# Kernel tuning notes

Measured on AMD Instinct MI355X. Metric: run time of the kernel, lower is better.

The kernel has to match this reference:

```python
import jax, jax.numpy as jnp
from jax import lax
import numpy as np

EPS = 1e-12      # F.normalize eps
TOP_N = 250      # top negatives selected
SMOOTH = 1e-5    # soft dice smooth


def _dilate10(m):
    # == 10 iterations of 3x3x3 binary max-pool dilation. m: [B,D,H,W] float.
    for _ in range(10):
        m = lax.reduce_window(m, 0.0, lax.max, (1, 3, 3, 3), (1, 1, 1, 1), 'SAME')
    return m


def _self_loss(feature, lab):
    # feature: [B,C,D,H,W], lab: [B,D,H,W] int
    feat = jnp.moveaxis(feature, 1, -1)                       # [B,D,H,W,C]
    pos = (lab == 1)
    posf = pos.astype(feat.dtype)
    cnt = posf.sum()
    std = (feat * posf[..., None]).sum((0, 1, 2, 3)) / jnp.maximum(cnt, 1.0)
    std = jnp.where(cnt > 0, std, 0.0)                        # [C]
    std_n = std / jnp.maximum(jnp.linalg.norm(std), EPS)
    feat_n = feat / jnp.maximum(jnp.linalg.norm(feat, axis=-1, keepdims=True), EPS)
    # cosine similarity of per-voxel normalized features vs normalized mean positive
    sim = jnp.einsum('bdhwc,c->bdhw', feat_n, std_n)

    # positive term: mean over positives of (1 - sim)
    pos_loss = jnp.where(cnt > 0, ((1.0 - sim) * posf).sum() / jnp.maximum(cnt, 1.0), 0.0)

    # easily-misclassified ring: dilate(pos,10) & ~pos; mean relu(sim)
    mis = (_dilate10(posf) > 0) & (~pos)
    misf = mis.astype(sim.dtype)
    mcnt = misf.sum()
    mis_loss = jnp.where(mcnt > 0, (jax.nn.relu(sim) * misf).sum() / jnp.maximum(mcnt, 1.0), 0.0)

    # hard negatives: top-250 sims among label==0, scatter to mask, dilate, & ~pos
    neg = (lab == 0)
    neg_sims = jnp.where(neg, sim, -jnp.inf).reshape(-1)
    top_vals, top_idx = lax.top_k(neg_sims, TOP_N)
    hsm = jnp.zeros(neg_sims.shape[0], sim.dtype).at[top_idx].set(
        jnp.where(jnp.isfinite(top_vals), 1.0, 0.0)).reshape(sim.shape)
    fin = (_dilate10(hsm) > 0) & (~pos)
    finf = fin.astype(sim.dtype)
    fcnt = finf.sum()
    neg_loss = jnp.where(fcnt > 0, (jax.nn.relu(sim) * finf).sum() / jnp.maximum(fcnt, 1.0), 0.0)

    return pos_loss + mis_loss + neg_loss


def _ce_dice(net_output, target):
    lab = target[:, 0]                                        # [B,D,H,W]
    logp = jax.nn.log_softmax(net_output, axis=1)
    ce = -jnp.mean(jnp.take_along_axis(logp, target, axis=1))
    probs = jnp.exp(logp)                                     # softmax_helper_dim1
    nc = net_output.shape[1]
    onehot = jax.nn.one_hot(lab, nc, axis=1, dtype=probs.dtype)  # [B,nc,D,H,W]
    axes = (0, 2, 3, 4)                                       # batch_dice=True
    tp = (probs * onehot).sum(axes)
    fp = (probs * (1.0 - onehot)).sum(axes)
    fn = ((1.0 - probs) * onehot).sum(axes)
    dc = (2.0 * tp + SMOOTH) / (2.0 * tp + fp + fn + SMOOTH + 1e-8)
    dice = -jnp.mean(dc[1:])                                  # do_bg=False
    return ce, dice


def reference(feature, net_output, target):
    ce, dice = _ce_dice(net_output, target)
    sl = _self_loss(feature, target[:, 0])
    return 1.0 * ce + 1.0 * dice + 5.0 * sl


def setup_inputs():
    key = jax.random.key(0)
    k1, k2, k3 = jax.random.split(key, 3)
    B, C, D, H, W = 2, 32, 64, 128, 128
    NC = 2
    feature = jax.random.normal(k1, (B, C, D, H, W), jnp.float32)
    net_output = jax.random.normal(k2, (B, NC, D, H, W), jnp.float32)
    target = jax.random.randint(k3, (B, 1, D, H, W), 0, 2).astype(jnp.int32)
    return {'feature': feature, 'net_output': net_output, 'target': target}
```

## Files before the change

kernel.cpp:

```cpp
#include <hip/hip_runtime.h>
#include <stdint.h>

typedef unsigned int u32;
typedef unsigned long long u64;
typedef float f4v __attribute__((ext_vector_type(4)));
typedef int i4v __attribute__((ext_vector_type(4)));

#define BB 2
#define CC 32
#define DD 64
#define HH 128
#define WW 128
#define SS (DD*HH*WW)
#define NN (BB*SS)
#define NQ (NN/4)
#define NWORDS (NN/64)
#define EPSF 1e-12f
#define TOPN 250u

struct Ctrl {
  u32 done4, tie, pad0, pad1;
};

struct Acc {
  double ce, tp, fp, fn;
  double stdsum[CC];
  double pos_num, mis_num, fin_num;
  u64 cnt, mcnt, fcnt;
};

__device__ __forceinline__ float waveRedF(float v){
#pragma unroll
  for (int o = 32; o; o >>= 1) v += __shfl_xor(v, o);
  return v;
}
__device__ __forceinline__ u32 waveRedU(u32 v){
#pragma unroll
  for (int o = 32; o; o >>= 1) v += __shfl_xor(v, o);
  return v;
}
__device__ __forceinline__ void red_d(double* dst, float v, volatile float* sh){
  int lane = threadIdx.x & 63, wid = threadIdx.x >> 6;
  v = waveRedF(v);
  if (lane == 0) sh[wid] = v;
  __syncthreads();
  if (threadIdx.x == 0){
    float t = 0.f;
    for (int i = 0; i < (int)(blockDim.x >> 6); i++) t += sh[i];
    atomicAdd(dst, (double)t);
  }
  __syncthreads();
}
__device__ __forceinline__ void red_u(u64* dst, u32 v, volatile u32* sh){
  int lane = threadIdx.x & 63, wid = threadIdx.x >> 6;
  v = waveRedU(v);
  if (lane == 0) sh[wid] = v;
  __syncthreads();
  if (threadIdx.x == 0){
    u32 t = 0;
    for (int i = 0; i < (int)(blockDim.x >> 6); i++) t += sh[i];
    atomicAdd(dst, (u64)t);
  }
  __syncthreads();
}

__device__ __forceinline__ u32 sortkey(float f){
  u32 u = __float_as_uint(f);
  return (u & 0x80000000u) ? ~u : (u | 0x80000000u);
}

__device__ __forceinline__ void select_top(const u32* __restrict__ hist, u32 nbins,
                                           u32 k, u32* shres, u32* binOut, u32* kremOut){
  __syncthreads();
  if (threadIdx.x < 64){
    int lane = threadIdx.x;
    u32 running = 0; bool found = false;
    for (u32 chunk = 0; chunk * 64 < nbins && !found; chunk++){
      int bin = (int)nbins - 1 - (int)(chunk * 64 + (u32)lane);
      u32 val = (bin >= 0) ? hist[bin] : 0u;
      u32 p = val;
#pragma unroll
      for (int o = 1; o < 64; o <<= 1){ u32 t = __shfl_up(p, o); if (lane >= o) p += t; }
      u32 tot = __shfl(p, 63);
      u32 incl = running + p, excl = incl - val;
      bool hit = (excl < k) && (incl >= k);
      u64 mb = __ballot(hit);
      if (mb){
        int hl = __ffsll((unsigned long long)mb) - 1;
        if (lane == hl){ shres[0] = (u32)bin; shres[1] = k - excl; }
        found = true;
      } else running += tot;
    }
    if (!found && lane == 0){ shres[0] = 0; shres[1] = k; }
  }
  __syncthreads();
  *binOut = shres[0]; *kremOut = shres[1];
}

__global__ __launch_bounds__(256) void k_pre(const int* __restrict__ tgt,
                                             u64* __restrict__ pbits,
                                             u32* __restrict__ cntArr,
                                             u32* __restrict__ zptr, u32 zwords){
  __shared__ u32 nibsh[256];
  __shared__ u32 shu[4];
  if (blockIdx.x == 0){
    for (u32 i = threadIdx.x; i < zwords; i += 256u) zptr[i] = 0;
  }
  u32 cnt = 0;
#pragma unroll 1
  for (u32 it = 0; it < 4; it++){
    u32 q = blockIdx.x * 1024u + it * 256u + threadIdx.x;
    i4v l4 = __builtin_nontemporal_load((const i4v*)(tgt + q * 4u));
    u32 nib = (l4.x ? 1u : 0u) | (l4.y ? 2u : 0u) | (l4.z ? 4u : 0u) | (l4.w ? 8u : 0u);
    cnt += __popc(nib);
    __syncthreads();
    nibsh[threadIdx.x] = nib;
    __syncthreads();
    if (threadIdx.x < 16){
      u64 o = 0;
#pragma unroll
      for (int j = 0; j < 16; j++)
        o |= (u64)(nibsh[threadIdx.x * 16 + j] & 0xFu) << (4 * j);
      pbits[blockIdx.x * 64u + it * 16u + threadIdx.x] = o;
    }
  }
  int lane = threadIdx.x & 63, wid = threadIdx.x >> 6;
  cnt = waveRedU(cnt);
  if (lane == 0) shu[wid] = cnt;
  __syncthreads();
  if (threadIdx.x == 0) cntArr[blockIdx.x] = shu[0] + shu[1] + shu[2] + shu[3];
}

__global__ __launch_bounds__(256) void k_ce_std(const float* __restrict__ feat,
                                                const float* __restrict__ net,
                                                const u64* __restrict__ pbits, Acc* acc){
  __shared__ float sh[16];
  if (blockIdx.x < 64u){
    u32 bid = blockIdx.x;
    float ce = 0.f, tp = 0.f, fp = 0.f, fnn = 0.f;
#pragma unroll 1
    for (u32 it = 0; it < 32; it++){
      u32 q = bid * 8192u + it * 256u + threadIdx.x;
      u32 nib = (u32)(pbits[q >> 4] >> ((q & 15u) << 2)) & 0xFu;
      u32 v = q * 4u;
      u32 b = v >> 20, s = v & (SS - 1);
      const float* nb = net + (size_t)(b * 2) * SS + s;
      f4v x0 = __builtin_nontemporal_load((const f4v*)(nb));
      f4v x1 = __builtin_nontemporal_load((const f4v*)(nb + SS));
      float xs0[4] = {x0.x, x0.y, x0.z, x0.w};
      float xs1[4] = {x1.x, x1.y, x1.z, x1.w};
#pragma unroll
      for (int j = 0; j < 4; j++){
        int lab = (nib >> j) & 1;
        float m = fmaxf(xs0[j], xs1[j]);
        float lse = m + logf(expf(xs0[j] - m) + expf(xs1[j] - m));
        ce += lse - (lab ? xs1[j] : xs0[j]);
        float p1 = expf(xs1[j] - lse);
        if (lab){ tp += p1; fnn += 1.0f - p1; } else fp += p1;
      }
    }
    int lane = threadIdx.x & 63, wid = threadIdx.x >> 6;
    ce = waveRedF(ce); tp = waveRedF(tp); fp = waveRedF(fp); fnn = waveRedF(fnn);
    if (lane == 0){ sh[wid] = ce; sh[4 + wid] = tp; sh[8 + wid] = fp; sh[12 + wid] = fnn; }
    __syncthreads();
    if (threadIdx.x == 0){
      atomicAdd(&acc->ce, (double)(sh[0] + sh[1] + sh[2] + sh[3]));
      atomicAdd(&acc->tp, (double)(sh[4] + sh[5] + sh[6] + sh[7]));
      atomicAdd(&acc->fp, (double)(sh[8] + sh[9] + sh[10] + sh[11]));
      atomicAdd(&acc->fn, (double)(sh[12] + sh[13] + sh[14] + sh[15]));
    }
  } else {
    u32 bx = blockIdx.x - 64u;
    u32 c = bx & 31u;
    u32 chunk = bx >> 5;
    u32 vbase = chunk * 65536u;
    u32 b = vbase >> 20;
    u32 s0 = vbase & (SS - 1);
    const float* fp_ = feat + (size_t)b * CC * SS + (size_t)c * SS + s0;
    const u64* pb = pbits + (vbase >> 6);
    float a = 0.f;
#pragma unroll 8
    for (u32 i = 0; i < 64; i++){
      u32 off = i * 1024u + threadIdx.x * 4u;
      float4 f = *(const float4*)(fp_ + off);
      u32 bits = (u32)(pb[off >> 6] >> (off & 63u)) & 0xFu;
      if (bits & 1u) a += f.x;
      if (bits & 2u) a += f.y;
      if (bits & 4u) a += f.z;
      if (bits & 8u) a += f.w;
    }
    int lane = threadIdx.x & 63, wid = threadIdx.x >> 6;
    a = waveRedF(a);
    if (lane == 0) sh[wid] = a;
    __syncthreads();
    if (threadIdx.x == 0)
      atomicAdd(&acc->stdsum[c], (double)(sh[0] + sh[1] + sh[2] + sh[3]));
  }
}

__global__ __launch_bounds__(256) void k_sim(const float* __restrict__ feat,
                                             const u64* __restrict__ pbits,
                                             const u32* __restrict__ cntArr,
                                             Acc* acc, float* __restrict__ sim,
                                             u32* __restrict__ h1){
  __shared__ float st[CC];
  __shared__ u32 lh[2048];
  __shared__ float shf[4];
  __shared__ u32 scnt;
  if (threadIdx.x < 64){
    u32 sc = 0;
#pragma unroll
    for (int i = 0; i < 8; i++) sc += cntArr[threadIdx.x * 8 + i];
    sc = waveRedU(sc);
    if (threadIdx.x == 0) scnt = sc;
  }
  __syncthreads();
  u32 cnt = scnt;
  if (blockIdx.x == 0 && threadIdx.x == 0) acc->cnt = (u64)cnt;
  {
    float sv = 0.f;
    if (threadIdx.x < CC && cnt) sv = (float)(acc->stdsum[threadIdx.x] / (double)cnt);
    if (threadIdx.x < 64){
      float t = waveRedF(sv * sv);
      float d = fmaxf(sqrtf(t), EPSF);
      if (threadIdx.x < CC) st[threadIdx.x] = sv / d;
    }
  }
  for (u32 i = threadIdx.x; i < 2048u; i += 256u) lh[i] = 0;
  __syncthreads();
  u32 vbase = (511u - blockIdx.x) * 4096u;
  u32 b = vbase >> 20;
  u32 s0 = vbase & (SS - 1);
  const float* fp = feat + (size_t)b * CC * SS + s0;
  float4 dt[4], n2[4];
#pragma unroll
  for (int g = 0; g < 4; g++){
    dt[g].x = dt[g].y = dt[g].z = dt[g].w = 0.f;
    n2[g].x = n2[g].y = n2[g].z = n2[g].w = 0.f;
  }
#pragma unroll 2
  for (u32 c = 0; c < CC; c++){
    float w = st[c];
    const float* fc = fp + (size_t)c * SS;
    float4 f[4];
#pragma unroll
    for (int g = 0; g < 4; g++)
      f[g] = *(const float4*)(fc + (u32)g * 1024u + threadIdx.x * 4u);
#pragma unroll
    for (int g = 0; g < 4; g++){
      dt[g].x += f[g].x * w; dt[g].y += f[g].y * w;
      dt[g].z += f[g].z * w; dt[g].w += f[g].w * w;
      n2[g].x += f[g].x * f[g].x; n2[g].y += f[g].y * f[g].y;
      n2[g].z += f[g].z * f[g].z; n2[g].w += f[g].w * f[g].w;
    }
  }
  float pn = 0.f;
#pragma unroll
  for (int g = 0; g < 4; g++){
    u32 off = (u32)g * 1024u + threadIdx.x * 4u;
    u32 v = vbase + off;
    float4 sm;
    sm.x = dt[g].x / fmaxf(sqrtf(n2[g].x), EPSF);
    sm.y = dt[g].y / fmaxf(sqrtf(n2[g].y), EPSF);
    sm.z = dt[g].z / fmaxf(sqrtf(n2[g].z), EPSF);
    sm.w = dt[g].w / fmaxf(sqrtf(n2[g].w), EPSF);
    *(float4*)(sim + v) = sm;
    u32 bits = (u32)(pbits[v >> 6] >> (v & 63u)) & 0xFu;
    float ss[4] = {sm.x, sm.y, sm.z, sm.w};
#pragma unroll
    for (int j = 0; j < 4; j++){
      if ((bits >> j) & 1u) pn += 1.f - ss[j];
      else atomicAdd(&lh[sortkey(ss[j]) >> 21], 1u);
    }
  }
  __syncthreads();
  for (u32 i = threadIdx.x; i < 2048u; i += 256u)
    if (lh[i]) atomicAdd(&h1[i], lh[i]);
  red_d(&acc->pos_num, pn, shf);
}

__device__ __forceinline__ void dilwh_slab(const u64* __restrict__ in, u64* __restrict__ out,
                                           u32 slab, u64* arr){
  u32 base = slab * 256u;
  int t = threadIdx.x;
  if (t < 128){
    u64 lo = in[base + 2 * t], hi = in[base + 2 * t + 1];
    u64 al = lo, ah = hi;
#pragma unroll
    for (int i = 0; i < 10; i++){ u64 c = al >> 63; ah = ah | (ah << 1) | c; al = al | (al << 1); }
    u64 bl = lo, bh = hi;
#pragma unroll
    for (int i = 0; i < 10; i++){ u64 c = bh << 63; bl = bl | (bl >> 1) | c; bh = bh | (bh >> 1); }
    arr[2 * t] = al | bl;
    arr[2 * t + 1] = ah | bh;
  }
  __syncthreads();
  int h = t >> 1, wj = t & 1;
  int h0 = h - 10 > 0 ? h - 10 : 0;
  int h1 = h + 10 < 127 ? h + 10 : 127;
  u64 o = 0;
  for (int hh = h0; hh <= h1; hh++) o |= arr[2 * hh + wj];
  out[base + (u32)t] = o;
  __syncthreads();
}

__global__ __launch_bounds__(256) void k_dilwh(const u64* __restrict__ in, u64* __restrict__ out){
  __shared__ u64 arr[256];
  dilwh_slab(in, out, blockIdx.x, arr);
}

__global__ __launch_bounds__(256) void k_histL2(const float* __restrict__ sim,
                                                const u64* __restrict__ pbits,
                                                const u32* __restrict__ h1,
                                                u32* __restrict__ h2,
                                                const u64* __restrict__ P,
                                                u64* __restrict__ T1P){
  __shared__ u64 arr[256];
  __shared__ u32 lh[2048];
  __shared__ u32 shres[2];
  if (blockIdx.x < 128u) dilwh_slab(P, T1P, blockIdx.x, arr);
  u32 p1, k1;
  select_top(h1, 2048, TOPN, shres, &p1, &k1);
  for (u32 i = threadIdx.x; i < 2048u; i += 256u) lh[i] = 0;
  __syncthreads();
  const u32 stride = 512u * 256u;
#pragma unroll 1
  for (u32 it = 0; it < 4; it++){
    u32 q = blockIdx.x * 256u + threadIdx.x + it * stride;
    u32 nib = (u32)(pbits[q >> 4] >> ((q & 15u) << 2)) & 0xFu;
    float4 s4 = *(const float4*)(sim + q * 4u);
    float ss[4] = {s4.x, s4.y, s4.z, s4.w};
#pragma unroll
    for (int j = 0; j < 4; j++){
      if (!((nib >> j) & 1u)){
        u32 key = sortkey(ss[j]);
        if ((key >> 21) == p1) atomicAdd(&lh[(key >> 10) & 2047u], 1u);
      }
    }
  }
  __syncthreads();
  for (u32 i = threadIdx.x; i < 2048u; i += 256u)
    if (lh[i]) atomicAdd(&h2[i], lh[i]);
}

__global__ __launch_bounds__(256) void k_mark(const float* __restrict__ sim,
                                              const u64* __restrict__ pbits,
                                              u64* __restrict__ hs,
                                              const u32* __restrict__ h1,
                                              const u32* __restrict__ h2,
                                              Ctrl* ctrl){
  __shared__ u32 shres[2];
  u32 p1, k1, b2, k2;
  select_top(h1, 2048, TOPN, shres, &p1, &k1);
  select_top(h2, 2048, k1, shres, &b2, &k2);
  u32 p12 = (p1 << 11) | b2;
  int lane = threadIdx.x & 63;
  const u32 stride = 1024u * 256u;
#pragma unroll 1
  for (u32 it = 0; it < 8; it++){
    u32 v = blockIdx.x * 256u + threadIdx.x + it * stride;
    u64 w = pbits[v >> 6];
    bool neg = !((w >> (v & 63u)) & 1ull);
    bool seed = false;
    if (neg){
      u32 pref = sortkey(sim[v]) >> 10;
      if (pref > p12) seed = true;
      else if (pref == p12){
        u32 old = atomicAdd(&ctrl->tie, 1u);
        if (old < k2) seed = true;
      }
    }
    u64 mb = __ballot(seed);
    if (lane == 0) hs[v >> 6] = mb;
  }
}

__global__ __launch_bounds__(256) void k_final(const float* __restrict__ sim,
                                               const u64* __restrict__ P,
                                               const u64* __restrict__ T1P,
                                               const u64* __restrict__ T1H,
                                               Acc* acc, Ctrl* ctrl, float* out){
  __shared__ float shf[4]; __shared__ u32 shu[4];
  __shared__ int amLast;
  u32 wi = blockIdx.x * 256u + threadIdx.x;
  u32 wj = wi & 1u;
  u32 row = wi >> 1;
  int h = (int)(row & 127u);
  int d = (int)((row >> 7) & 63u);
  u32 b = row >> 13;
  int d0 = d - 10 > 0 ? d - 10 : 0;
  int d1 = d + 10 < 63 ? d + 10 : 63;
  const u64* bp = T1P + ((size_t)(b << 13) + (u32)h) * 2 + wj;
  const u64* bh = T1H + ((size_t)(b << 13) + (u32)h) * 2 + wj;
  u64 dpw = 0, dhw = 0;
  for (int dd = d0; dd <= d1; dd++){
    dpw |= bp[(size_t)dd * 256];
    dhw |= bh[(size_t)dd * 256];
  }
  u64 pw = P[wi];
  u64 mis = dpw & ~pw;
  u64 fin = dhw & ~pw;
  float mn = 0.f, fnm = 0.f;
  u32 mc = (u32)__popcll(mis), fc = (u32)__popcll(fin);
  const float* sp = sim + (size_t)wi * 64u;
#pragma unroll 1
  for (int jj = 0; jj < 16; jj++){
    float4 s4 = *(const float4*)(sp + jj * 4);
    float ss[4] = {s4.x, s4.y, s4.z, s4.w};
#pragma unroll
    for (int j = 0; j < 4; j++){
      int bit = jj * 4 + j;
      float r = fmaxf(ss[j], 0.f);
      if ((mis >> bit) & 1ull) mn += r;
      if ((fin >> bit) & 1ull) fnm += r;
    }
  }
  red_d(&acc->mis_num, mn, shf);
  red_d(&acc->fin_num, fnm, shf);
  red_u(&acc->mcnt, mc, shu);
  red_u(&acc->fcnt, fc, shu);
  __threadfence();
  if (threadIdx.x == 0) amLast = (atomicAdd(&ctrl->done4, 1u) == gridDim.x - 1);
  __syncthreads();
  if (amLast && threadIdx.x == 0){
    double ce = acc->ce / (double)NN;
    double tp = acc->tp, fp = acc->fp, fn = acc->fn;
    double dc1 = (2.0 * tp + 1e-5) / (2.0 * tp + fp + fn + 1e-5 + 1e-8);
    u64 cnt = acc->cnt;
    double pos_loss = cnt ? (acc->pos_num / (double)cnt) : 0.0;
    u64 mcnt = atomicAdd(&acc->mcnt, 0ull);
    u64 fcnt = atomicAdd(&acc->fcnt, 0ull);
    double mis_loss = mcnt ? (atomicAdd(&acc->mis_num, 0.0) / (double)mcnt) : 0.0;
    double neg_loss = fcnt ? (atomicAdd(&acc->fin_num, 0.0) / (double)fcnt) : 0.0;
    out[0] = (float)(ce - dc1 + 5.0 * (pos_loss + mis_loss + neg_loss));
  }
}

extern "C" void kernel_launch(void* const* d_in, const int* in_sizes, int n_in,
                              void* d_out, int out_size, void* d_ws, size_t ws_size,
                              hipStream_t stream){
  (void)in_sizes; (void)n_in; (void)out_size; (void)ws_size;
  const float* feat = (const float*)d_in[0];
  const float* net  = (const float*)d_in[1];
  const int*   tgt  = (const int*)d_in[2];
  float* out = (float*)d_out;
  char* ws = (char*)d_ws;

  size_t off = 0;
  auto take = [&](size_t bytes) -> void* {
    void* p = (void*)(ws + off);
    off += (bytes + 255) & ~(size_t)255;
    return p;
  };
  float* sim = (float*)take((size_t)NN * 4);
  u64* P   = (u64*)take((size_t)NWORDS * 8);
  u64* T1P = (u64*)take((size_t)NWORDS * 8);
  u64* HS  = (u64*)take((size_t)NWORDS * 8);
  u64* T1H = (u64*)take((size_t)NWORDS * 8);
  u32* cntArr = (u32*)take(512 * 4);
  size_t zstart = off;
  u32* h1 = (u32*)take(2048 * 4);
  u32* h2 = (u32*)take(2048 * 4);
  Ctrl* ctrl = (Ctrl*)take(sizeof(Ctrl));
  Acc* acc = (Acc*)take(sizeof(Acc));
  u32 zwords = (u32)((off - zstart) >> 2);

  k_pre<<<512, 256, 0, stream>>>(tgt, P, cntArr, (u32*)(ws + zstart), zwords);
  k_ce_std<<<1088, 256, 0, stream>>>(feat, net, P, acc);
  k_sim<<<512, 256, 0, stream>>>(feat, P, cntArr, acc, sim, h1);
  k_histL2<<<512, 256, 0, stream>>>(sim, P, h1, h2, P, T1P);
  k_mark<<<1024, 256, 0, stream>>>(sim, P, HS, h1, h2, ctrl);
  k_dilwh<<<128, 256, 0, stream>>>(HS, T1H);
  k_final<<<128, 256, 0, stream>>>(sim, P, T1P, T1H, acc, ctrl, out);
}
```

Baseline: 487.0 us.

## Fuse sim, histogram, mark, dilate and final stages into one persistent kernel with grid barriers

```diff
diff --git a/kernel.cpp b/kernel.cpp
--- a/kernel.cpp
+++ b/kernel.cpp
@@ -19,7 +19,7 @@
 #define TOPN 250u
 
 struct Ctrl {
-  u32 done4, tie, pad0, pad1;
+  u32 done4, tie, bar0, bar1, bar2, bar3, pad0, pad1;
 };
 
 struct Acc {
@@ -69,7 +69,19 @@
   return (u & 0x80000000u) ? ~u : (u | 0x80000000u);
 }
 
-__device__ __forceinline__ void select_top(const u32* __restrict__ hist, u32 nbins,
+__device__ __forceinline__ void gridbar(u32* bar, u32 n){
+  __syncthreads();
+  __threadfence();
+  if (threadIdx.x == 0){
+    __hip_atomic_fetch_add(bar, 1u, __ATOMIC_ACQ_REL, __HIP_MEMORY_SCOPE_AGENT);
+    while (__hip_atomic_load(bar, __ATOMIC_ACQUIRE, __HIP_MEMORY_SCOPE_AGENT) < n)
+      __builtin_amdgcn_s_sleep(2);
+  }
+  __syncthreads();
+  __threadfence();
+}
+
+__device__ __forceinline__ void select_top(u32* __restrict__ hist, u32 nbins,
                                            u32 k, u32* shres, u32* binOut, u32* kremOut){
   __syncthreads();
   if (threadIdx.x < 64){
@@ -77,7 +89,8 @@
     u32 running = 0; bool found = false;
     for (u32 chunk = 0; chunk * 64 < nbins && !found; chunk++){
       int bin = (int)nbins - 1 - (int)(chunk * 64 + (u32)lane);
-      u32 val = (bin >= 0) ? hist[bin] : 0u;
+      u32 val = (bin >= 0) ?
+        __hip_atomic_load(&hist[bin], __ATOMIC_RELAXED, __HIP_MEMORY_SCOPE_AGENT) : 0u;
       u32 p = val;
 #pragma unroll
       for (int o = 1; o < 64; o <<= 1){ u32 t = __shfl_up(p, o); if (lane >= o) p += t; }
@@ -95,6 +108,31 @@
   }
   __syncthreads();
   *binOut = shres[0]; *kremOut = shres[1];
+}
+
+__device__ __forceinline__ void dilwh_slab(const u64* __restrict__ in, u64* __restrict__ out,
+                                           u32 slab, u64* arr){
+  u32 base = slab * 256u;
+  int t = threadIdx.x;
+  if (t < 128){
+    u64 lo = in[base + 2 * t], hi = in[base + 2 * t + 1];
+    u64 al = lo, ah = hi;
+#pragma unroll
+    for (int i = 0; i < 10; i++){ u64 c = al >> 63; ah = ah | (ah << 1) | c; al = al | (al << 1); }
+    u64 bl = lo, bh = hi;
+#pragma unroll
+    for (int i = 0; i < 10; i++){ u64 c = bh << 63; bl = bl | (bl >> 1) | c; bh = bh | (bh >> 1); }
+    arr[2 * t] = al | bl;
+    arr[2 * t + 1] = ah | bh;
+  }
+  __syncthreads();
+  int h = t >> 1, wj = t & 1;
+  int h0 = h - 10 > 0 ? h - 10 : 0;
+  int h1 = h + 10 < 127 ? h + 10 : 127;
+  u64 o = 0;
+  for (int hh = h0; hh <= h1; hh++) o |= arr[2 * hh + wj];
+  out[base + (u32)t] = o;
+  __syncthreads();
 }
 
 __global__ __launch_bounds__(256) void k_pre(const int* __restrict__ tgt,
@@ -198,15 +236,25 @@
   }
 }
 
-__global__ __launch_bounds__(256) void k_sim(const float* __restrict__ feat,
-                                             const u64* __restrict__ pbits,
-                                             const u32* __restrict__ cntArr,
-                                             Acc* acc, float* __restrict__ sim,
-                                             u32* __restrict__ h1){
+__global__ __launch_bounds__(256, 2) void k_simtail(const float* __restrict__ feat,
+                                                    const u64* __restrict__ pbits,
+                                                    const u32* __restrict__ cntArr,
+                                                    Acc* acc, float* __restrict__ sim,
+                                                    u32* __restrict__ h1,
+                                                    u32* __restrict__ h2,
+                                                    u64* __restrict__ T1P,
+                                                    u64* __restrict__ hs,
+                                                    u64* __restrict__ T1H,
+                                                    Ctrl* ctrl, float* out){
   __shared__ float st[CC];
   __shared__ u32 lh[2048];
+  __shared__ u64 arr[256];
+  __shared__ u32 shres[2];
   __shared__ float shf[4];
+  __shared__ u32 shu[4];
   __shared__ u32 scnt;
+  __shared__ int amLast;
+
   if (threadIdx.x < 64){
     u32 sc = 0;
 #pragma unroll
@@ -216,7 +264,8 @@
   }
   __syncthreads();
   u32 cnt = scnt;
-  if (blockIdx.x == 0 && threadIdx.x == 0) acc->cnt = (u64)cnt;
+  if (blockIdx.x == 0 && threadIdx.x == 0)
+    __hip_atomic_store(&acc->cnt, (u64)cnt, __ATOMIC_RELAXED, __HIP_MEMORY_SCOPE_AGENT);
   {
     float sv = 0.f;
     if (threadIdx.x < CC && cnt) sv = (float)(acc->stdsum[threadIdx.x] / (double)cnt);
@@ -228,211 +277,171 @@
   }
   for (u32 i = threadIdx.x; i < 2048u; i += 256u) lh[i] = 0;
   __syncthreads();
-  u32 vbase = (511u - blockIdx.x) * 4096u;
-  u32 b = vbase >> 20;
-  u32 s0 = vbase & (SS - 1);
-  const float* fp = feat + (size_t)b * CC * SS + s0;
-  float4 dt[4], n2[4];
-#pragma unroll
-  for (int g = 0; g < 4; g++){
-    dt[g].x = dt[g].y = dt[g].z = dt[g].w = 0.f;
-    n2[g].x = n2[g].y = n2[g].z = n2[g].w = 0.f;
-  }
+
+  {
+    u32 vbase = (511u - blockIdx.x) * 4096u;
+    u32 b = vbase >> 20;
+    u32 s0 = vbase & (SS - 1);
+    const float* fp = feat + (size_t)b * CC * SS + s0;
+    float4 dt[4], n2[4];
+#pragma unroll
+    for (int g = 0; g < 4; g++){
+      dt[g].x = dt[g].y = dt[g].z = dt[g].w = 0.f;
+      n2[g].x = n2[g].y = n2[g].z = n2[g].w = 0.f;
+    }
 #pragma unroll 2
-  for (u32 c = 0; c < CC; c++){
-    float w = st[c];
-    const float* fc = fp + (size_t)c * SS;
-    float4 f[4];
-#pragma unroll
-    for (int g = 0; g < 4; g++)
-      f[g] = *(const float4*)(fc + (u32)g * 1024u + threadIdx.x * 4u);
+    for (u32 c = 0; c < CC; c++){
+      float w = st[c];
+      const float* fc = fp + (size_t)c * SS;
+      float4 f[4];
+#pragma unroll
+      for (int g = 0; g < 4; g++)
+        f[g] = *(const float4*)(fc + (u32)g * 1024u + threadIdx.x * 4u);
+#pragma unroll
+      for (int g = 0; g < 4; g++){
+        dt[g].x += f[g].x * w; dt[g].y += f[g].y * w;
+        dt[g].z += f[g].z * w; dt[g].w += f[g].w * w;
+        n2[g].x += f[g].x * f[g].x; n2[g].y += f[g].y * f[g].y;
+        n2[g].z += f[g].z * f[g].z; n2[g].w += f[g].w * f[g].w;
+      }
+    }
+    float pn = 0.f;
 #pragma unroll
     for (int g = 0; g < 4; g++){
-      dt[g].x += f[g].x * w; dt[g].y += f[g].y * w;
-      dt[g].z += f[g].z * w; dt[g].w += f[g].w * w;
-      n2[g].x += f[g].x * f[g].x; n2[g].y += f[g].y * f[g].y;
-      n2[g].z += f[g].z * f[g].z; n2[g].w += f[g].w * f[g].w;
-    }
-  }
-  float pn = 0.f;
-#pragma unroll
-  for (int g = 0; g < 4; g++){
-    u32 off = (u32)g * 1024u + threadIdx.x * 4u;
-    u32 v = vbase + off;
-    float4 sm;
-    sm.x = dt[g].x / fmaxf(sqrtf(n2[g].x), EPSF);
-    sm.y = dt[g].y / fmaxf(sqrtf(n2[g].y), EPSF);
-    sm.z = dt[g].z / fmaxf(sqrtf(n2[g].z), EPSF);
-    sm.w = dt[g].w / fmaxf(sqrtf(n2[g].w), EPSF);
-    *(float4*)(sim + v) = sm;
-    u32 bits = (u32)(pbits[v >> 6] >> (v & 63u)) & 0xFu;
-    float ss[4] = {sm.x, sm.y, sm.z, sm.w};
-#pragma unroll
-    for (int j = 0; j < 4; j++){
-      if ((bits >> j) & 1u) pn += 1.f - ss[j];
-      else atomicAdd(&lh[sortkey(ss[j]) >> 21], 1u);
-    }
-  }
-  __syncthreads();
-  for (u32 i = threadIdx.x; i < 2048u; i += 256u)
-    if (lh[i]) atomicAdd(&h1[i], lh[i]);
-  red_d(&acc->pos_num, pn, shf);
-}
-
-__device__ __forceinline__ void dilwh_slab(const u64* __restrict__ in, u64* __restrict__ out,
-                                           u32 slab, u64* arr){
-  u32 base = slab * 256u;
-  int t = threadIdx.x;
-  if (t < 128){
-    u64 lo = in[base + 2 * t], hi = in[base + 2 * t + 1];
-    u64 al = lo, ah = hi;
-#pragma unroll
-    for (int i = 0; i < 10; i++){ u64 c = al >> 63; ah = ah | (ah << 1) | c; al = al | (al << 1); }
-    u64 bl = lo, bh = hi;
-#pragma unroll
-    for (int i = 0; i < 10; i++){ u64 c = bh << 63; bl = bl | (bl >> 1) | c; bh = bh | (bh >> 1); }
-    arr[2 * t] = al | bl;
-    arr[2 * t + 1] = ah | bh;
-  }
-  __syncthreads();
-  int h = t >> 1, wj = t & 1;
-  int h0 = h - 10 > 0 ? h - 10 : 0;
-  int h1 = h + 10 < 127 ? h + 10 : 127;
-  u64 o = 0;
-  for (int hh = h0; hh <= h1; hh++) o |= arr[2 * hh + wj];
-  out[base + (u32)t] = o;
-  __syncthreads();
-}
-
-__global__ __launch_bounds__(256) void k_dilwh(const u64* __restrict__ in, u64* __restrict__ out){
-  __shared__ u64 arr[256];
-  dilwh_slab(in, out, blockIdx.x, arr);
-}
-
-__global__ __launch_bounds__(256) void k_histL2(const float* __restrict__ sim,
-                                                const u64* __restrict__ pbits,
-                                                const u32* __restrict__ h1,
-                                                u32* __restrict__ h2,
-                                                const u64* __restrict__ P,
-                                                u64* __restrict__ T1P){
-  __shared__ u64 arr[256];
-  __shared__ u32 lh[2048];
-  __shared__ u32 shres[2];
-  if (blockIdx.x < 128u) dilwh_slab(P, T1P, blockIdx.x, arr);
-  u32 p1, k1;
-  select_top(h1, 2048, TOPN, shres, &p1, &k1);
-  for (u32 i = threadIdx.x; i < 2048u; i += 256u) lh[i] = 0;
-  __syncthreads();
-  const u32 stride = 512u * 256u;
+      u32 off = (u32)g * 1024u + threadIdx.x * 4u;
+      u32 v = vbase + off;
+      float4 sm;
+      sm.x = dt[g].x / fmaxf(sqrtf(n2[g].x), EPSF);
+      sm.y = dt[g].y / fmaxf(sqrtf(n2[g].y), EPSF);
+      sm.z = dt[g].z / fmaxf(sqrtf(n2[g].z), EPSF);
+      sm.w = dt[g].w / fmaxf(sqrtf(n2[g].w), EPSF);
+      *(float4*)(sim + v) = sm;
+      u32 bits = (u32)(pbits[v >> 6] >> (v & 63u)) & 0xFu;
+      float ss[4] = {sm.x, sm.y, sm.z, sm.w};
+#pragma unroll
+      for (int j = 0; j < 4; j++){
+        if ((bits >> j) & 1u) pn += 1.f - ss[j];
+        else atomicAdd(&lh[sortkey(ss[j]) >> 21], 1u);
+      }
+    }
+    __syncthreads();
+    for (u32 i = threadIdx.x; i < 2048u; i += 256u)
+      if (lh[i]) atomicAdd(&h1[i], lh[i]);
+    red_d(&acc->pos_num, pn, shf);
+  }
+  gridbar(&ctrl->bar0, 512u);
+
+  {
+    if (blockIdx.x < 128u) dilwh_slab(pbits, T1P, blockIdx.x, arr);
+    u32 p1, k1;
+    select_top(h1, 2048, TOPN, shres, &p1, &k1);
+    for (u32 i = threadIdx.x; i < 2048u; i += 256u) lh[i] = 0;
+    __syncthreads();
+    const u32 stride = 512u * 256u;
 #pragma unroll 1
-  for (u32 it = 0; it < 4; it++){
-    u32 q = blockIdx.x * 256u + threadIdx.x + it * stride;
-    u32 nib = (u32)(pbits[q >> 4] >> ((q & 15u) << 2)) & 0xFu;
-    float4 s4 = *(const float4*)(sim + q * 4u);
-    float ss[4] = {s4.x, s4.y, s4.z, s4.w};
-#pragma unroll
-    for (int j = 0; j < 4; j++){
-      if (!((nib >> j) & 1u)){
-        u32 key = sortkey(ss[j]);
-        if ((key >> 21) == p1) atomicAdd(&lh[(key >> 10) & 2047u], 1u);
-      }
-    }
-  }
-  __syncthreads();
-  for (u32 i = threadIdx.x; i < 2048u; i += 256u)
-    if (lh[i]) atomicAdd(&h2[i], lh[i]);
-}
-
-__global__ __launch_bounds__(256) void k_mark(const float* __restrict__ sim,
-                                              const u64* __restrict__ pbits,
-                                              u64* __restrict__ hs,
-                                              const u32* __restrict__ h1,
-                                              const u32* __restrict__ h2,
-                                              Ctrl* ctrl){
-  __shared__ u32 shres[2];
-  u32 p1, k1, b2, k2;
-  select_top(h1, 2048, TOPN, shres, &p1, &k1);
-  select_top(h2, 2048, k1, shres, &b2, &k2);
-  u32 p12 = (p1 << 11) | b2;
-  int lane = threadIdx.x & 63;
-  const u32 stride = 1024u * 256u;
+    for (u32 it = 0; it < 4; it++){
+      u32 q = blockIdx.x * 256u + threadIdx.x + it * stride;
+      u32 nib = (u32)(pbits[q >> 4] >> ((q & 15u) << 2)) & 0xFu;
+      float4 s4 = *(const float4*)(sim + q * 4u);
+      float ss[4] = {s4.x, s4.y, s4.z, s4.w};
+#pragma unroll
+      for (int j = 0; j < 4; j++){
+        if (!((nib >> j) & 1u)){
+          u32 key = sortkey(ss[j]);
+          if ((key >> 21) == p1) atomicAdd(&lh[(key >> 10) & 2047u], 1u);
+        }
+      }
+    }
+    __syncthreads();
+    for (u32 i = threadIdx.x; i < 2048u; i += 256u)
+      if (lh[i]) atomicAdd(&h2[i], lh[i]);
+  }
+  gridbar(&ctrl->bar1, 512u);
+
+  {
+    u32 p1, k1, b2, k2;
+    select_top(h1, 2048, TOPN, shres, &p1, &k1);
+    select_top(h2, 2048, k1, shres, &b2, &k2);
+    u32 p12 = (p1 << 11) | b2;
+    int lane = threadIdx.x & 63;
+    const u32 stride = 512u * 256u;
 #pragma unroll 1
-  for (u32 it = 0; it < 8; it++){
-    u32 v = blockIdx.x * 256u + threadIdx.x + it * stride;
-    u64 w = pbits[v >> 6];
-    bool neg = !((w >> (v & 63u)) & 1ull);
-    bool seed = false;
-    if (neg){
-      u32 pref = sortkey(sim[v]) >> 10;
-      if (pref > p12) seed = true;
-      else if (pref == p12){
-        u32 old = atomicAdd(&ctrl->tie, 1u);
-        if (old < k2) seed = true;
-      }
-    }
-    u64 mb = __ballot(seed);
-    if (lane == 0) hs[v >> 6] = mb;
-  }
-}
-
-__global__ __launch_bounds__(256) void k_final(const float* __restrict__ sim,
-                                               const u64* __restrict__ P,
-                                               const u64* __restrict__ T1P,
-                                               const u64* __restrict__ T1H,
-                                               Acc* acc, Ctrl* ctrl, float* out){
-  __shared__ float shf[4]; __shared__ u32 shu[4];
-  __shared__ int amLast;
-  u32 wi = blockIdx.x * 256u + threadIdx.x;
-  u32 wj = wi & 1u;
-  u32 row = wi >> 1;
-  int h = (int)(row & 127u);
-  int d = (int)((row >> 7) & 63u);
-  u32 b = row >> 13;
-  int d0 = d - 10 > 0 ? d - 10 : 0;
-  int d1 = d + 10 < 63 ? d + 10 : 63;
-  const u64* bp = T1P + ((size_t)(b << 13) + (u32)h) * 2 + wj;
-  const u64* bh = T1H + ((size_t)(b << 13) + (u32)h) * 2 + wj;
-  u64 dpw = 0, dhw = 0;
-  for (int dd = d0; dd <= d1; dd++){
-    dpw |= bp[(size_t)dd * 256];
-    dhw |= bh[(size_t)dd * 256];
-  }
-  u64 pw = P[wi];
-  u64 mis = dpw & ~pw;
-  u64 fin = dhw & ~pw;
-  float mn = 0.f, fnm = 0.f;
-  u32 mc = (u32)__popcll(mis), fc = (u32)__popcll(fin);
-  const float* sp = sim + (size_t)wi * 64u;
+    for (u32 it = 0; it < 16; it++){
+      u32 v = blockIdx.x * 256u + threadIdx.x + it * stride;
+      u64 w = pbits[v >> 6];
+      bool neg = !((w >> (v & 63u)) & 1ull);
+      bool seed = false;
+      if (neg){
+        u32 pref = sortkey(sim[v]) >> 10;
+        if (pref > p12) seed = true;
+        else if (pref == p12){
+          u32 old = atomicAdd(&ctrl->tie, 1u);
+          if (old < k2) seed = true;
+        }
+      }
+      u64 mb = __ballot(seed);
+      if (lane == 0) hs[v >> 6] = mb;
+    }
+  }
+  gridbar(&ctrl->bar2, 512u);
+
+  if (blockIdx.x < 128u) dilwh_slab(hs, T1H, blockIdx.x, arr);
+  gridbar(&ctrl->bar3, 512u);
+  if (blockIdx.x >= 128u) return;
+
+  {
+    u32 wi = blockIdx.x * 256u + threadIdx.x;
+    u32 wj = wi & 1u;
+    u32 row = wi >> 1;
+    int h = (int)(row & 127u);
+    int d = (int)((row >> 7) & 63u);
+    u32 b = row >> 13;
+    int d0 = d - 10 > 0 ? d - 10 : 0;
+    int d1 = d + 10 < 63 ? d + 10 : 63;
+    const u64* bp = T1P + ((size_t)(b << 13) + (u32)h) * 2 + wj;
+    const u64* bh = T1H + ((size_t)(b << 13) + (u32)h) * 2 + wj;
+    u64 dpw = 0, dhw = 0;
+    for (int dd = d0; dd <= d1; dd++){
+      dpw |= bp[(size_t)dd * 256];
+      dhw |= bh[(size_t)dd * 256];
+    }
+    u64 pw = pbits[wi];
+    u64 mis = dpw & ~pw;
+    u64 fin = dhw & ~pw;
+    float mn = 0.f, fnm = 0.f;
+    u32 mc = (u32)__popcll(mis), fc = (u32)__popcll(fin);
+    const float* sp = sim + (size_t)wi * 64u;
 #pragma unroll 1
-  for (int jj = 0; jj < 16; jj++){
-    float4 s4 = *(const float4*)(sp + jj * 4);
-    float ss[4] = {s4.x, s4.y, s4.z, s4.w};
-#pragma unroll
-    for (int j = 0; j < 4; j++){
-      int bit = jj * 4 + j;
-      float r = fmaxf(ss[j], 0.f);
-      if ((mis >> bit) & 1ull) mn += r;
-      if ((fin >> bit) & 1ull) fnm += r;
-    }
-  }
-  red_d(&acc->mis_num, mn, shf);
-  red_d(&acc->fin_num, fnm, shf);
-  red_u(&acc->mcnt, mc, shu);
-  red_u(&acc->fcnt, fc, shu);
-  __threadfence();
-  if (threadIdx.x == 0) amLast = (atomicAdd(&ctrl->done4, 1u) == gridDim.x - 1);
-  __syncthreads();
-  if (amLast && threadIdx.x == 0){
-    double ce = acc->ce / (double)NN;
-    double tp = acc->tp, fp = acc->fp, fn = acc->fn;
-    double dc1 = (2.0 * tp + 1e-5) / (2.0 * tp + fp + fn + 1e-5 + 1e-8);
-    u64 cnt = acc->cnt;
-    double pos_loss = cnt ? (acc->pos_num / (double)cnt) : 0.0;
-    u64 mcnt = atomicAdd(&acc->mcnt, 0ull);
-    u64 fcnt = atomicAdd(&acc->fcnt, 0ull);
-    double mis_loss = mcnt ? (atomicAdd(&acc->mis_num, 0.0) / (double)mcnt) : 0.0;
-    double neg_loss = fcnt ? (atomicAdd(&acc->fin_num, 0.0) / (double)fcnt) : 0.0;
-    out[0] = (float)(ce - dc1 + 5.0 * (pos_loss + mis_loss + neg_loss));
+    for (int jj = 0; jj < 16; jj++){
+      float4 s4 = *(const float4*)(sp + jj * 4);
+      float ss[4] = {s4.x, s4.y, s4.z, s4.w};
+#pragma unroll
+      for (int j = 0; j < 4; j++){
+        int bit = jj * 4 + j;
+        float r = fmaxf(ss[j], 0.f);
+        if ((mis >> bit) & 1ull) mn += r;
+        if ((fin >> bit) & 1ull) fnm += r;
+      }
+    }
+    red_d(&acc->mis_num, mn, shf);
+    red_d(&acc->fin_num, fnm, shf);
+    red_u(&acc->mcnt, mc, shu);
+    red_u(&acc->fcnt, fc, shu);
+    __threadfence();
+    if (threadIdx.x == 0) amLast = (atomicAdd(&ctrl->done4, 1u) == 127u);
+    __syncthreads();
+    if (amLast && threadIdx.x == 0){
+      double ce = acc->ce / (double)NN;
+      double tp = acc->tp, fp = acc->fp, fn = acc->fn;
+      double dc1 = (2.0 * tp + 1e-5) / (2.0 * tp + fp + fn + 1e-5 + 1e-8);
+      u64 cnt2 = acc->cnt;
+      double pos_loss = cnt2 ? (atomicAdd(&acc->pos_num, 0.0) / (double)cnt2) : 0.0;
+      u64 mcnt = atomicAdd(&acc->mcnt, 0ull);
+      u64 fcnt = atomicAdd(&acc->fcnt, 0ull);
+      double mis_loss = mcnt ? (atomicAdd(&acc->mis_num, 0.0) / (double)mcnt) : 0.0;
+      double neg_loss = fcnt ? (atomicAdd(&acc->fin_num, 0.0) / (double)fcnt) : 0.0;
+      out[0] = (float)(ce - dc1 + 5.0 * (pos_loss + mis_loss + neg_loss));
+    }
   }
 }
 
@@ -467,9 +476,5 @@
 
   k_pre<<<512, 256, 0, stream>>>(tgt, P, cntArr, (u32*)(ws + zstart), zwords);
   k_ce_std<<<1088, 256, 0, stream>>>(feat, net, P, acc);
-  k_sim<<<512, 256, 0, stream>>>(feat, P, cntArr, acc, sim, h1);
-  k_histL2<<<512, 256, 0, stream>>>(sim, P, h1, h2, P, T1P);
-  k_mark<<<1024, 256, 0, stream>>>(sim, P, HS, h1, h2, ctrl);
-  k_dilwh<<<128, 256, 0, stream>>>(HS, T1H);
-  k_final<<<128, 256, 0, stream>>>(sim, P, T1P, T1H, acc, ctrl, out);
-}
+  k_simtail<<<512, 256, 0, stream>>>(feat, P, cntArr, acc, sim, h1, h2, T1P, HS, T1H, ctrl, out);
+}
```

Result: slower. 847.3 us (+74.0%).

## Fuse seed marking with W/H dilation and move positive-mask dilation earlier

Applied to the files above, without the earlier changes.

```diff
diff --git a/kernel.cpp b/kernel.cpp
--- a/kernel.cpp
+++ b/kernel.cpp
@@ -95,6 +95,55 @@
   }
   __syncthreads();
   *binOut = shres[0]; *kremOut = shres[1];
+}
+
+__device__ __forceinline__ void dilwh_lds(const u64* hsw, u64* __restrict__ out,
+                                          u32 slab, u64* arr){
+  int t = threadIdx.x;
+  if (t < 128){
+    u64 lo = hsw[2 * t], hi = hsw[2 * t + 1];
+    u64 al = lo, ah = hi;
+#pragma unroll
+    for (int i = 0; i < 10; i++){ u64 c = al >> 63; ah = ah | (ah << 1) | c; al = al | (al << 1); }
+    u64 bl = lo, bh = hi;
+#pragma unroll
+    for (int i = 0; i < 10; i++){ u64 c = bh << 63; bl = bl | (bl >> 1) | c; bh = bh | (bh >> 1); }
+    arr[2 * t] = al | bl;
+    arr[2 * t + 1] = ah | bh;
+  }
+  __syncthreads();
+  int h = t >> 1, wj = t & 1;
+  int h0 = h - 10 > 0 ? h - 10 : 0;
+  int h1 = h + 10 < 127 ? h + 10 : 127;
+  u64 o = 0;
+  for (int hh = h0; hh <= h1; hh++) o |= arr[2 * hh + wj];
+  out[slab * 256u + (u32)t] = o;
+  __syncthreads();
+}
+
+__device__ __forceinline__ void dilwh_slab(const u64* __restrict__ in, u64* __restrict__ out,
+                                           u32 slab, u64* arr){
+  u32 base = slab * 256u;
+  int t = threadIdx.x;
+  if (t < 128){
+    u64 lo = in[base + 2 * t], hi = in[base + 2 * t + 1];
+    u64 al = lo, ah = hi;
+#pragma unroll
+    for (int i = 0; i < 10; i++){ u64 c = al >> 63; ah = ah | (ah << 1) | c; al = al | (al << 1); }
+    u64 bl = lo, bh = hi;
+#pragma unroll
+    for (int i = 0; i < 10; i++){ u64 c = bh << 63; bl = bl | (bl >> 1) | c; bh = bh | (bh >> 1); }
+    arr[2 * t] = al | bl;
+    arr[2 * t + 1] = ah | bh;
+  }
+  __syncthreads();
+  int h = t >> 1, wj = t & 1;
+  int h0 = h - 10 > 0 ? h - 10 : 0;
+  int h1 = h + 10 < 127 ? h + 10 : 127;
+  u64 o = 0;
+  for (int hh = h0; hh <= h1; hh++) o |= arr[2 * hh + wj];
+  out[base + (u32)t] = o;
+  __syncthreads();
 }
 
 __global__ __launch_bounds__(256) void k_pre(const int* __restrict__ tgt,
@@ -133,8 +182,10 @@
 
 __global__ __launch_bounds__(256) void k_ce_std(const float* __restrict__ feat,
                                                 const float* __restrict__ net,
-                                                const u64* __restrict__ pbits, Acc* acc){
+                                                const u64* __restrict__ pbits,
+                                                u64* __restrict__ T1P, Acc* acc){
   __shared__ float sh[16];
+  __shared__ u64 arr[256];
   if (blockIdx.x < 64u){
     u32 bid = blockIdx.x;
     float ce = 0.f, tp = 0.f, fp = 0.f, fnn = 0.f;
@@ -169,7 +220,7 @@
       atomicAdd(&acc->fp, (double)(sh[8] + sh[9] + sh[10] + sh[11]));
       atomicAdd(&acc->fn, (double)(sh[12] + sh[13] + sh[14] + sh[15]));
     }
-  } else {
+  } else if (blockIdx.x < 1088u){
     u32 bx = blockIdx.x - 64u;
     u32 c = bx & 31u;
     u32 chunk = bx >> 5;
@@ -195,6 +246,8 @@
     __syncthreads();
     if (threadIdx.x == 0)
       atomicAdd(&acc->stdsum[c], (double)(sh[0] + sh[1] + sh[2] + sh[3]));
+  } else {
+    dilwh_slab(pbits, T1P, blockIdx.x - 1088u, arr);
   }
 }
 
@@ -228,7 +281,7 @@
   }
   for (u32 i = threadIdx.x; i < 2048u; i += 256u) lh[i] = 0;
   __syncthreads();
-  u32 vbase = (511u - blockIdx.x) * 4096u;
+  u32 vbase = blockIdx.x * 4096u;
   u32 b = vbase >> 20;
   u32 s0 = vbase & (SS - 1);
   const float* fp = feat + (size_t)b * CC * SS + s0;
@@ -279,46 +332,12 @@
   red_d(&acc->pos_num, pn, shf);
 }
 
-__device__ __forceinline__ void dilwh_slab(const u64* __restrict__ in, u64* __restrict__ out,
-                                           u32 slab, u64* arr){
-  u32 base = slab * 256u;
-  int t = threadIdx.x;
-  if (t < 128){
-    u64 lo = in[base + 2 * t], hi = in[base + 2 * t + 1];
-    u64 al = lo, ah = hi;
-#pragma unroll
-    for (int i = 0; i < 10; i++){ u64 c = al >> 63; ah = ah | (ah << 1) | c; al = al | (al << 1); }
-    u64 bl = lo, bh = hi;
-#pragma unroll
-    for (int i = 0; i < 10; i++){ u64 c = bh << 63; bl = bl | (bl >> 1) | c; bh = bh | (bh >> 1); }
-    arr[2 * t] = al | bl;
-    arr[2 * t + 1] = ah | bh;
-  }
-  __syncthreads();
-  int h = t >> 1, wj = t & 1;
-  int h0 = h - 10 > 0 ? h - 10 : 0;
-  int h1 = h + 10 < 127 ? h + 10 : 127;
-  u64 o = 0;
-  for (int hh = h0; hh <= h1; hh++) o |= arr[2 * hh + wj];
-  out[base + (u32)t] = o;
-  __syncthreads();
-}
-
-__global__ __launch_bounds__(256) void k_dilwh(const u64* __restrict__ in, u64* __restrict__ out){
-  __shared__ u64 arr[256];
-  dilwh_slab(in, out, blockIdx.x, arr);
-}
-
-__global__ __launch_bounds__(256) void k_histL2(const float* __restrict__ sim,
-                                                const u64* __restrict__ pbits,
-                                                const u32* __restrict__ h1,
-                                                u32* __restrict__ h2,
-                                                const u64* __restrict__ P,
-                                                u64* __restrict__ T1P){
-  __shared__ u64 arr[256];
+__global__ __launch_bounds__(256) void k_hist2(const float* __restrict__ sim,
+                                               const u64* __restrict__ pbits,
+                                               const u32* __restrict__ h1,
+                                               u32* __restrict__ h2){
   __shared__ u32 lh[2048];
   __shared__ u32 shres[2];
-  if (blockIdx.x < 128u) dilwh_slab(P, T1P, blockIdx.x, arr);
   u32 p1, k1;
   select_top(h1, 2048, TOPN, shres, &p1, &k1);
   for (u32 i = threadIdx.x; i < 2048u; i += 256u) lh[i] = 0;
@@ -343,24 +362,27 @@
     if (lh[i]) atomicAdd(&h2[i], lh[i]);
 }
 
-__global__ __launch_bounds__(256) void k_mark(const float* __restrict__ sim,
-                                              const u64* __restrict__ pbits,
-                                              u64* __restrict__ hs,
-                                              const u32* __restrict__ h1,
-                                              const u32* __restrict__ h2,
-                                              Ctrl* ctrl){
+__global__ __launch_bounds__(256) void k_markdil(const float* __restrict__ sim,
+                                                 const u64* __restrict__ pbits,
+                                                 const u32* __restrict__ h1,
+                                                 const u32* __restrict__ h2,
+                                                 u64* __restrict__ T1H,
+                                                 Ctrl* ctrl){
   __shared__ u32 shres[2];
+  __shared__ u64 hsw[256];
+  __shared__ u64 arr[256];
   u32 p1, k1, b2, k2;
   select_top(h1, 2048, TOPN, shres, &p1, &k1);
   select_top(h2, 2048, k1, shres, &b2, &k2);
   u32 p12 = (p1 << 11) | b2;
-  int lane = threadIdx.x & 63;
-  const u32 stride = 1024u * 256u;
-#pragma unroll 1
-  for (u32 it = 0; it < 8; it++){
-    u32 v = blockIdx.x * 256u + threadIdx.x + it * stride;
-    u64 w = pbits[v >> 6];
-    bool neg = !((w >> (v & 63u)) & 1ull);
+  int lane = threadIdx.x & 63, wid = threadIdx.x >> 6;
+  u32 slab = blockIdx.x;
+#pragma unroll 4
+  for (u32 i = 0; i < 64; i++){
+    u32 w = (u32)wid * 64u + i;
+    u32 v = slab * 16384u + w * 64u + (u32)lane;
+    u64 pw = pbits[v >> 6];
+    bool neg = !((pw >> (v & 63u)) & 1ull);
     bool seed = false;
     if (neg){
       u32 pref = sortkey(sim[v]) >> 10;
@@ -371,8 +393,10 @@
       }
     }
     u64 mb = __ballot(seed);
-    if (lane == 0) hs[v >> 6] = mb;
-  }
+    if (lane == 0) hsw[w] = mb;
+  }
+  __syncthreads();
+  dilwh_lds(hsw, T1H, slab, arr);
 }
 
 __global__ __launch_bounds__(256) void k_final(const float* __restrict__ sim,
@@ -455,7 +479,6 @@
   float* sim = (float*)take((size_t)NN * 4);
   u64* P   = (u64*)take((size_t)NWORDS * 8);
   u64* T1P = (u64*)take((size_t)NWORDS * 8);
-  u64* HS  = (u64*)take((size_t)NWORDS * 8);
   u64* T1H = (u64*)take((size_t)NWORDS * 8);
   u32* cntArr = (u32*)take(512 * 4);
   size_t zstart = off;
@@ -466,10 +489,9 @@
   u32 zwords = (u32)((off - zstart) >> 2);
 
   k_pre<<<512, 256, 0, stream>>>(tgt, P, cntArr, (u32*)(ws + zstart), zwords);
-  k_ce_std<<<1088, 256, 0, stream>>>(feat, net, P, acc);
+  k_ce_std<<<1216, 256, 0, stream>>>(feat, net, P, T1P, acc);
   k_sim<<<512, 256, 0, stream>>>(feat, P, cntArr, acc, sim, h1);
-  k_histL2<<<512, 256, 0, stream>>>(sim, P, h1, h2, P, T1P);
-  k_mark<<<1024, 256, 0, stream>>>(sim, P, HS, h1, h2, ctrl);
-  k_dilwh<<<128, 256, 0, stream>>>(HS, T1H);
+  k_hist2<<<512, 256, 0, stream>>>(sim, P, h1, h2);
+  k_markdil<<<128, 256, 0, stream>>>(sim, P, h1, h2, T1H, ctrl);
   k_final<<<128, 256, 0, stream>>>(sim, P, T1P, T1H, acc, ctrl, out);
 }
```

Result: slower. 510.5 us (+4.8%).
